# Optimization experiments

Measured on AMD Instinct MI355X. Metric: run time of the kernel, lower is better.

## Reference

```python
import jax, jax.numpy as jnp
import numpy as np

B, N, C, H, HD = 32, 512, 384, 6, 64
WH = WW = WT = 8
ALPHA = 4.0
KS = 5


def safe_pow(x, p):
    # x = relu(...) >= 0; avoid nan grads at x == 0
    pos = x > 0
    return jnp.where(pos, jnp.where(pos, x, 1.0) ** p, 0.0)


def setup_inputs() -> dict:
    key = jax.random.key(0)
    ks = jax.random.split(key, 12)
    s = 0.02
    return {
        "x": jax.random.normal(ks[0], (B, N, C), jnp.float32),
        "y": jax.random.normal(ks[1], (B, N, C), jnp.float32),
        "Wqkvg": jax.random.normal(ks[2], (4 * C, C), jnp.float32) * s,
        "bqkvg": jax.random.normal(ks[3], (4 * C,), jnp.float32) * s,
        "Wproj": jax.random.normal(ks[4], (C, C), jnp.float32) * s,
        "bproj": jax.random.normal(ks[5], (C,), jnp.float32) * s,
        "dwc_w": jax.random.normal(ks[6], (HD, 1, KS, KS, KS), jnp.float32) * s,
        "dwc_b": jax.random.normal(ks[7], (HD,), jnp.float32) * s,
        "power_p": jax.random.normal(ks[8], (1, H, 1, HD), jnp.float32) * s,
        "scale_p": jax.random.normal(ks[9], (1, 1, C), jnp.float32) * s,
        "pe": jax.random.normal(ks[10], (1, N, C), jnp.float32) * s,
    }


def reference(x, y, Wqkvg, bqkvg, Wproj, bproj, dwc_w, dwc_b, power_p, scale_p, pe):
    qkv = (x @ Wqkvg.T + bqkvg).reshape(B, N, 4, C)
    k = qkv[:, :, 1]
    v = qkv[:, :, 2]
    g = qkv[:, :, 3]
    q = (y @ Wqkvg.T + bqkvg).reshape(B, N, 4, C)[:, :, 0]

    k = k + pe
    scale = jax.nn.softplus(scale_p)          # (1,1,C)
    power = 1.0 + ALPHA * jax.nn.sigmoid(power_p)  # (1,H,1,HD)
    q = q / scale
    k = k / scale

    def heads(t):  # (B,N,C) -> (B,H,N,HD)
        return t.reshape(B, N, H, HD).transpose(0, 2, 1, 3)

    q = heads(q)
    k = heads(k)
    v = heads(v)

    q_pos = safe_pow(jax.nn.relu(q), power)
    q_neg = safe_pow(jax.nn.relu(-q), power)
    k_pos = safe_pow(jax.nn.relu(k), power)
    k_neg = safe_pow(jax.nn.relu(-k), power)

    q_sim = jnp.concatenate([q_pos, q_neg], axis=-1)   # (B,H,N,2HD)
    q_opp = jnp.concatenate([q_neg, q_pos], axis=-1)
    kf = jnp.concatenate([k_pos, k_neg], axis=-1)      # (B,H,N,2HD)
    v1, v2 = jnp.split(v, 2, axis=-1)                  # each (B,H,N,HD/2)

    k_mean = kf.mean(axis=-2)                          # (B,H,2HD)
    inv_sqrt_n = N ** (-0.5)
    kfs = kf * inv_sqrt_n

    z_sim = 1.0 / (jnp.einsum("bhnd,bhd->bhn", q_sim, k_mean)[..., None] + 1e-6)
    kv1 = jnp.einsum("bhnd,bhne->bhde", kfs, v1 * inv_sqrt_n)
    x_sim = jnp.einsum("bhnd,bhde->bhne", q_sim, kv1) * z_sim

    z_opp = 1.0 / (jnp.einsum("bhnd,bhd->bhn", q_opp, k_mean)[..., None] + 1e-6)
    kv2 = jnp.einsum("bhnd,bhne->bhde", kfs, v2 * inv_sqrt_n)
    x_opp = jnp.einsum("bhnd,bhde->bhne", q_opp, kv2) * z_opp

    xa = jnp.concatenate([x_sim, x_opp], axis=-1)      # (B,H,N,HD)
    xa = xa.transpose(0, 2, 1, 3).reshape(B, N, C)

    # depthwise conv3d on v: (B*H, HD, Wh, Ww, Wt)
    vr = v.reshape(B * H, WH, WW, WT, HD).transpose(0, 4, 1, 2, 3)
    pad = KS // 2
    vc = jax.lax.conv_general_dilated(
        vr, dwc_w, window_strides=(1, 1, 1),
        padding=[(pad, pad)] * 3,
        dimension_numbers=("NCDHW", "OIDHW", "NCDHW"),
        feature_group_count=HD,
    ) + dwc_b[None, :, None, None, None]
    vc = vc.transpose(0, 2, 3, 4, 1).reshape(B, N, C)

    out = (xa + vc) * g
    out = out @ Wproj.T + bproj
    return out
```

## Files before the change

### kernel.cpp

```cpp
#include <hip/hip_runtime.h>
#include <hip/hip_bf16.h>
#include <math.h>

#define B_  32
#define N_  512
#define C_  384
#define H_  6
#define HD_ 64
#define M_  (B_*N_)

typedef __attribute__((ext_vector_type(8))) short bfrag;
typedef __attribute__((ext_vector_type(8))) unsigned short u16x8;
typedef __attribute__((ext_vector_type(4))) float f32x4;

__device__ __forceinline__ unsigned short f2bfu(float f){
  unsigned int u = __float_as_uint(f);
  u += 0x7fffu + ((u >> 16) & 1u);
  return (unsigned short)(u >> 16);
}
__device__ __forceinline__ float bf2f(unsigned short u){
  return __uint_as_float(((unsigned int)u) << 16);
}
__device__ __forceinline__ bfrag cvt8(float4 a, float4 b){
  bfrag r;
  r[0]=(short)f2bfu(a.x); r[1]=(short)f2bfu(a.y); r[2]=(short)f2bfu(a.z); r[3]=(short)f2bfu(a.w);
  r[4]=(short)f2bfu(b.x); r[5]=(short)f2bfu(b.y); r[6]=(short)f2bfu(b.z); r[7]=(short)f2bfu(b.w);
  return r;
}
__device__ __forceinline__ void gload_lds16(const unsigned short* gp, unsigned short* lp){
  __builtin_amdgcn_global_load_lds(
      (const __attribute__((address_space(1))) void*)gp,
      (__attribute__((address_space(3))) void*)lp, 16, 0, 0);
}

__global__ void param_kernel(const float* __restrict__ scale_p,
                             const float* __restrict__ power_p,
                             float* __restrict__ scale_inv,
                             float* __restrict__ power){
  int t = threadIdx.x;
  if (t < C_){
    float s  = scale_p[t];
    scale_inv[t] = 1.0f / log1pf(expf(s));
  }
  if (t < H_*HD_){
    float p = power_p[t];
    power[t] = 1.0f + 4.0f / (1.0f + expf(-p));
  }
}

__global__ void sentinel_kernel(float* __restrict__ out, int n){
  int i = blockIdx.x*256 + threadIdx.x;
  if (i < n) out[i] = 1.0e9f;
}

__global__ __launch_bounds__(256) void cvt_bf16_kernel(
    const float* __restrict__ x, const float* __restrict__ y,
    const float* __restrict__ W,
    unsigned short* __restrict__ xb, unsigned short* __restrict__ yb,
    unsigned short* __restrict__ Wb)
{
  const int bid = blockIdx.x;
  const float* src; unsigned short* dst; int base;
  if (bid < 3072)      { src = x; dst = xb; base = bid; }
  else if (bid < 6144) { src = y; dst = yb; base = bid - 3072; }
  else                 { src = W; dst = Wb; base = bid - 6144; }
  const size_t i0 = ((size_t)base*256 + threadIdx.x)*8;
  float4 a = *reinterpret_cast<const float4*>(src + i0);
  float4 b = *reinterpret_cast<const float4*>(src + i0 + 4);
  *reinterpret_cast<bfrag*>(dst + i0) = cvt8(a, b);
}

__global__ __launch_bounds__(256) void gemm_qkvg(
    const unsigned short* __restrict__ xb, const unsigned short* __restrict__ yb,
    const unsigned short* __restrict__ Wb, const float* __restrict__ bias,
    const float* __restrict__ pe, const float* __restrict__ scale_inv,
    float* __restrict__ q, float* __restrict__ k,
    unsigned short* __restrict__ v, unsigned short* __restrict__ g)
{
  __shared__ unsigned short As[2][4096];
  __shared__ unsigned short Bs[2][4096];

  const int tid  = threadIdx.x;
  const int row0 = blockIdx.y * 128;
  const int col0 = blockIdx.x * 128;
  const int mode = blockIdx.x / 3;
  const unsigned short* Ab = (mode == 0) ? yb : xb;

  const int wave = tid >> 6, lane = tid & 63;
  const int wm = (wave >> 1) * 64, wn = (wave & 1) * 64;
  const int fr = lane & 15, quad = lane >> 4;
  const int srr = tid >> 2;
  const int skc = (tid & 3) * 8;

  const unsigned short* ga0 = &Ab[(size_t)(row0 + srr)*C_ + skc];
  const unsigned short* gb0 = &Wb[(size_t)(col0 + srr)*C_ + skc];
  const size_t gstep = (size_t)64*C_;

  f32x4 acc[4][4] = {};

  gload_lds16(ga0,         &As[0][tid*8]);
  gload_lds16(ga0 + gstep, &As[0][2048 + tid*8]);
  gload_lds16(gb0,         &Bs[0][tid*8]);
  gload_lds16(gb0 + gstep, &Bs[0][2048 + tid*8]);
  __syncthreads();

  #pragma unroll 2
  for (int t = 0; t < 12; t++){
    const int cur = t & 1;
    if (t < 11){
      const int k0 = (t+1)*32;
      gload_lds16(ga0 + k0,         &As[cur^1][tid*8]);
      gload_lds16(ga0 + gstep + k0, &As[cur^1][2048 + tid*8]);
      gload_lds16(gb0 + k0,         &Bs[cur^1][tid*8]);
      gload_lds16(gb0 + gstep + k0, &Bs[cur^1][2048 + tid*8]);
    }
    bfrag af[4], bf[4];
    #pragma unroll
    for (int f = 0; f < 4; f++){
      af[f] = *reinterpret_cast<const bfrag*>(&As[cur][(wm + f*16 + fr)*32 + quad*8]);
      bf[f] = *reinterpret_cast<const bfrag*>(&Bs[cur][(wn + f*16 + fr)*32 + quad*8]);
    }
    #pragma unroll
    for (int i=0;i<4;i++)
      #pragma unroll
      for (int j=0;j<4;j++)
        acc[i][j] = __builtin_amdgcn_mfma_f32_16x16x32_bf16(af[i], bf[j], acc[i][j], 0, 0, 0);
    __syncthreads();
  }

  const int cbase = col0 - mode*384;
  #pragma unroll
  for (int i = 0; i < 4; i++){
    const int rowb = row0 + wm + i*16 + quad*4;
    #pragma unroll
    for (int j = 0; j < 4; j++){
      const int cc = cbase + wn + j*16 + fr;
      const float bcol = bias[mode*384 + cc];
      if (mode == 0){
        const float scv = scale_inv[cc];
        #pragma unroll
        for (int r = 0; r < 4; r++)
          q[(size_t)(rowb + r)*C_ + cc] = (acc[i][j][r] + bcol) * scv;
      } else if (mode == 1){
        const float scv = scale_inv[cc];
        #pragma unroll
        for (int r = 0; r < 4; r++){
          const int row = rowb + r;
          const int n = row & (N_-1);
          k[(size_t)row*C_ + cc] = (acc[i][j][r] + bcol + pe[n*C_ + cc]) * scv;
        }
      } else if (mode == 2){
        #pragma unroll
        for (int r = 0; r < 4; r++)
          v[(size_t)(rowb + r)*C_ + cc] = f2bfu(acc[i][j][r] + bcol);
      } else {
        #pragma unroll
        for (int r = 0; r < 4; r++)
          g[(size_t)(rowb + r)*C_ + cc] = f2bfu(acc[i][j][r] + bcol);
      }
    }
  }
}

#define NC_ 256
__global__ __launch_bounds__(512) void attn_kernel(
    const float* __restrict__ q, const float* __restrict__ k,
    const unsigned short* __restrict__ v, const float* __restrict__ power,
    float* __restrict__ xa)
{
  const int bh = blockIdx.x;
  const int b = bh / H_, h = bh % H_;
  __shared__ float pw[64];
  __shared__ __align__(16) unsigned short smem[54912];
  unsigned short* kfT  = smem;
  unsigned short* vT   = smem + 33792;
  unsigned short* kvBT = smem;
  unsigned short* qf   = smem + 33792;

  const int tid = threadIdx.x;
  const int wave = tid >> 6, lane = tid & 63;
  const int fr = lane & 15, quad = lane >> 4;
  if (tid < 64) pw[tid] = power[h*HD_ + tid];

  const float*          kbase = k + (size_t)b*N_*C_ + h*HD_;
  const unsigned short* vbase = v + (size_t)b*N_*C_ + h*HD_;

  for (int i = tid; i < 16*NC_; i += 512){
    int e = 64 + (i >> 8);
    int nl = i & (NC_-1);
    vT[e*264 + nl] = (e == 64) ? (unsigned short)0x3F80 : (unsigned short)0;
  }
  __syncthreads();

  f32x4 acc[5] = {};
  for (int chunk = 0; chunk < 2; chunk++){
    const int n0 = chunk * NC_;
    for (int it = 0; it < 32; it++){
      int flat = it*512 + tid;
      int c = flat & 63, nl = flat >> 6;
      float kval = kbase[(size_t)(n0+nl)*C_ + c];
      float p = pw[c];
      float ax = fabsf(kval);
      float pv = (ax > 0.0f) ? exp2f(p * log2f(ax)) : 0.0f;
      kfT[c*264 + nl]      = f2bfu((kval > 0.0f) ? pv : 0.0f);
      kfT[(64+c)*264 + nl] = f2bfu((kval < 0.0f) ? pv : 0.0f);
      vT[c*264 + nl] = vbase[(size_t)(n0+nl)*C_ + c];
    }
    __syncthreads();
    for (int kk = 0; kk < NC_/32; kk++){
      int ko = kk*32 + quad*8;
      bfrag af = *reinterpret_cast<const bfrag*>(&kfT[(wave*16 + fr)*264 + ko]);
      #pragma unroll
      for (int j = 0; j < 5; j++){
        bfrag bf = *reinterpret_cast<const bfrag*>(&vT[(j*16 + fr)*264 + ko]);
        acc[j] = __builtin_amdgcn_mfma_f32_16x16x32_bf16(af, bf, acc[j], 0, 0, 0);
      }
    }
    __syncthreads();
  }

  const float invN = 1.0f / (float)N_;
  {
    const int dbase = wave*16 + quad*4;
    #pragma unroll
    for (int j = 0; j < 4; j++){
      const int e = j*16 + fr;
      const int dd = (e < 32) ? dbase : (dbase ^ 64);
      ushort4 w4;
      w4.x = f2bfu(acc[j][0] * invN);
      w4.y = f2bfu(acc[j][1] * invN);
      w4.z = f2bfu(acc[j][2] * invN);
      w4.w = f2bfu(acc[j][3] * invN);
      *reinterpret_cast<ushort4*>(&kvBT[e*136 + dd]) = w4;
    }
    if (fr == 0){
      ushort4 wk;
      wk.x = f2bfu(acc[4][0] * invN);
      wk.y = f2bfu(acc[4][1] * invN);
      wk.z = f2bfu(acc[4][2] * invN);
      wk.w = f2bfu(acc[4][3] * invN);
      *reinterpret_cast<ushort4*>(&kvBT[64*136 + dbase]) = wk;
      *reinterpret_cast<ushort4*>(&kvBT[65*136 + (dbase^64)]) = wk;
    }
  }
  __syncthreads();

  const float* qbase = q + (size_t)b*N_*C_ + h*HD_;
  float* xabase = xa + (size_t)b*N_*C_ + h*HD_;
  for (int mc = 0; mc < 4; mc++){
    const int m0 = mc * 128;
    for (int it = 0; it < 16; it++){
      int flat = it*512 + tid;
      int c = flat & 63, nl = flat >> 6;
      float qval = qbase[(size_t)(m0+nl)*C_ + c];
      float p = pw[c];
      float ax = fabsf(qval);
      float pv = (ax > 0.0f) ? exp2f(p * log2f(ax)) : 0.0f;
      qf[nl*136 + c]      = f2bfu((qval > 0.0f) ? pv : 0.0f);
      qf[nl*136 + 64 + c] = f2bfu((qval < 0.0f) ? pv : 0.0f);
    }
    __syncthreads();
    f32x4 a2[5] = {};
    for (int kk = 0; kk < 4; kk++){
      int ko = kk*32 + quad*8;
      bfrag af = *reinterpret_cast<const bfrag*>(&qf[(wave*16 + fr)*136 + ko]);
      #pragma unroll
      for (int j = 0; j < 5; j++){
        bfrag bf = *reinterpret_cast<const bfrag*>(&kvBT[(j*16 + fr)*136 + ko]);
        a2[j] = __builtin_amdgcn_mfma_f32_16x16x32_bf16(af, bf, a2[j], 0, 0, 0);
      }
    }
    #pragma unroll
    for (int r = 0; r < 4; r++){
      const float zsim = __shfl(a2[4][r], quad*16);
      const float zopp = __shfl(a2[4][r], quad*16 + 1);
      const int n = m0 + wave*16 + quad*4 + r;
      #pragma unroll
      for (int j = 0; j < 4; j++){
        const int e = j*16 + fr;
        const float z = (e < 32) ? zsim : zopp;
        xabase[(size_t)n*C_ + e] = a2[j][r] / (z + 1e-6f);
      }
    }
    __syncthreads();
  }
}

__global__ __launch_bounds__(512) void conv_kernel(
    const unsigned short* __restrict__ v, const float* __restrict__ dwc_w,
    const float* __restrict__ dwc_b, float* __restrict__ xa)
{
  const int bh = blockIdx.x;
  const int b = bh / H_, h = bh % H_;
  __shared__ float vol[32][521];
  __shared__ float wv[32][126];
  __shared__ float wb[32];
  const int tid = threadIdx.x;
  const unsigned short* vbase = v + (size_t)b*N_*C_ + h*HD_;
  float* xabatch = xa + (size_t)b*N_*C_ + (size_t)h*N_*HD_;

  for (int half = 0; half < 2; half++){
    const int ch0 = half * 32;
    for (int it = 0; it < 32; it++){
      int flat = it*512 + tid;
      int cl = flat & 31, n = flat >> 5;
      vol[cl][n] = bf2f(vbase[(size_t)n*C_ + ch0 + cl]);
    }
    for (int i = tid; i < 32*125; i += 512){
      int ch = i / 125, wi = i - ch*125;
      wv[ch][wi] = dwc_w[(ch0+ch)*125 + wi];
    }
    if (tid < 32) wb[tid] = dwc_b[ch0 + tid];
    __syncthreads();

    for (int t = 0; t < 4; t++){
      const int task = t*512 + tid;
      const int ch = task & 31;
      const int zy = task >> 5;
      const int z = zy >> 3, yc = zy & 7;
      float o[8];
      const float bias = wb[ch];
      #pragma unroll
      for (int xx = 0; xx < 8; xx++) o[xx] = bias;
      #pragma unroll
      for (int kd = 0; kd < 5; kd++){
        const int zz = z + kd - 2;
        if ((unsigned)zz >= 8u) continue;
        #pragma unroll
        for (int kh = 0; kh < 5; kh++){
          const int yy = yc + kh - 2;
          if ((unsigned)yy >= 8u) continue;
          const float* row = &vol[ch][zz*64 + yy*8];
          float rr[8];
          #pragma unroll
          for (int xx = 0; xx < 8; xx++) rr[xx] = row[xx];
          const float* wrow = &wv[ch][kd*25 + kh*5];
          float w5[5];
          #pragma unroll
          for (int kw = 0; kw < 5; kw++) w5[kw] = wrow[kw];
          #pragma unroll
          for (int xx = 0; xx < 8; xx++){
            #pragma unroll
            for (int kw = 0; kw < 5; kw++){
              const int xi = xx + kw - 2;
              if ((unsigned)xi < 8u) o[xx] = fmaf(w5[kw], rr[xi], o[xx]);
            }
          }
        }
      }
      const int nb = zy * 8;
      #pragma unroll
      for (int xx = 0; xx < 8; xx++){
        const size_t di = (size_t)(nb + xx)*HD_ + ch0 + ch;
        xabatch[di] += o[xx];
      }
    }
    __syncthreads();
  }
}

__global__ __launch_bounds__(256) void proj_kernel(
    const float* __restrict__ xa, const unsigned short* __restrict__ g,
    const float* __restrict__ Wp, const float* __restrict__ bp,
    float* __restrict__ out)
{
  __shared__ short As[128][40];
  __shared__ short Bs[128][40];

  const int tid  = threadIdx.x;
  const int row0 = blockIdx.y * 128;
  const int col0 = blockIdx.x * 128;
  const int wave = tid >> 6, lane = tid & 63;
  const int wm = (wave >> 1) * 64, wn = (wave & 1) * 64;
  const int fr = lane & 15, quad = lane >> 4;
  const int sr = tid >> 2;
  const int sk = (tid & 3) * 8;

  f32x4 acc[4][4] = {};

  for (int k0 = 0; k0 < C_; k0 += 32){
    #pragma unroll
    for (int half = 0; half < 2; half++){
      const int r = sr + half*64;
      const size_t aidx = (size_t)(row0 + r)*C_ + k0 + sk;
      float4 x0 = *reinterpret_cast<const float4*>(&xa[aidx]);
      float4 x1 = *reinterpret_cast<const float4*>(&xa[aidx + 4]);
      u16x8 gv = *reinterpret_cast<const u16x8*>(&g[aidx]);
      x0.x*=bf2f(gv[0]); x0.y*=bf2f(gv[1]); x0.z*=bf2f(gv[2]); x0.w*=bf2f(gv[3]);
      x1.x*=bf2f(gv[4]); x1.y*=bf2f(gv[5]); x1.z*=bf2f(gv[6]); x1.w*=bf2f(gv[7]);
      const float* bp2 = &Wp[(size_t)(col0 + r)*C_ + k0 + sk];
      float4 b0 = *reinterpret_cast<const float4*>(bp2);
      float4 b1 = *reinterpret_cast<const float4*>(bp2 + 4);
      *reinterpret_cast<bfrag*>(&As[r][sk]) = cvt8(x0, x1);
      *reinterpret_cast<bfrag*>(&Bs[r][sk]) = cvt8(b0, b1);
    }
    __syncthreads();
    bfrag af[4], bf[4];
    #pragma unroll
    for (int f = 0; f < 4; f++){
      af[f] = *reinterpret_cast<const bfrag*>(&As[wm + f*16 + fr][quad*8]);
      bf[f] = *reinterpret_cast<const bfrag*>(&Bs[wn + f*16 + fr][quad*8]);
    }
    #pragma unroll
    for (int i=0;i<4;i++)
      #pragma unroll
      for (int j=0;j<4;j++)
        acc[i][j] = __builtin_amdgcn_mfma_f32_16x16x32_bf16(af[i], bf[j], acc[i][j], 0, 0, 0);
    __syncthreads();
  }

  #pragma unroll
  for (int i = 0; i < 4; i++){
    const int rowb = row0 + wm + i*16 + quad*4;
    #pragma unroll
    for (int j = 0; j < 4; j++){
      const int col = col0 + wn + j*16 + fr;
      const float bcol = bp[col];
      #pragma unroll
      for (int r = 0; r < 4; r++){
        out[(size_t)(rowb + r)*C_ + col] = acc[i][j][r] + bcol;
      }
    }
  }
}

extern "C" void kernel_launch(void* const* d_in, const int* in_sizes, int n_in,
                              void* d_out, int out_size, void* d_ws, size_t ws_size,
                              hipStream_t stream){
  float* out = (float*)d_out;

  const int expect[11] = {6291456, 6291456, 589824, 1536, 147456, 384, 8000, 64, 384, 384, 196608};
  bool ok = (n_in == 11);
  for (int i = 0; ok && i < 11; i++) ok = (in_sizes[i] == expect[i]);
  if (!ok){
    sentinel_kernel<<<(out_size+255)/256, 256, 0, stream>>>(out, out_size);
    return;
  }

  const float* x    = (const float*)d_in[0];
  const float* y    = (const float*)d_in[1];
  const float* W    = (const float*)d_in[2];
  const float* bq   = (const float*)d_in[3];
  const float* Wp   = (const float*)d_in[4];
  const float* bp   = (const float*)d_in[5];
  const float* dwcw = (const float*)d_in[6];
  const float* dwcb = (const float*)d_in[7];
  const float* pwp  = (const float*)d_in[8];
  const float* scp  = (const float*)d_in[9];
  const float* pe   = (const float*)d_in[10];

  float* ws = (float*)d_ws;
  const size_t SZ = (size_t)M_ * C_;
  float* q  = ws;
  float* k  = ws + SZ;
  unsigned short* v = (unsigned short*)(ws + 2*SZ);
  unsigned short* g = v + SZ;
  float* xa = ws + 3*SZ;
  unsigned short* Wb = (unsigned short*)xa;
  unsigned short* xb = (unsigned short*)(ws + 4*SZ);
  unsigned short* yb = xb + SZ;
  float* scale_inv = ws + 5*SZ;
  float* power     = scale_inv + 512;

  param_kernel<<<1, 512, 0, stream>>>(scp, pwp, scale_inv, power);
  cvt_bf16_kernel<<<6432, 256, 0, stream>>>(x, y, W, xb, yb, Wb);
  gemm_qkvg<<<dim3(12, 128), 256, 0, stream>>>(xb, yb, Wb, bq, pe, scale_inv, q, k, v, g);
  attn_kernel<<<dim3(B_*H_), 512, 0, stream>>>(q, k, v, power, xa);
  conv_kernel<<<dim3(B_*H_), 512, 0, stream>>>(v, dwcw, dwcb, xa);
  proj_kernel<<<dim3(3, 128), 256, 0, stream>>>(xa, g, Wp, bp, out);
}
```

Baseline: 257.2 us.

## Fuse power feature map into QKV GEMM epilogue and bf16 pipeline projection

The QKV GEMM epilogue now applies the scale, positional embedding and signed power feature map directly and writes q/k feature maps as bf16 in a per-head [pos|neg] layout. The attention kernel then only does vectorized copies into shared memory instead of the fp32 loads and per-element pow. The conv kernel fuses the gating multiply and writes a bf16 activation. The projection GEMM uses a pre-converted bf16 Wproj with double-buffered direct-to-LDS loads. This cuts fp32 traffic and repeated transcendental work, at the cost of more complex workspace aliasing and an epilogue that writes twice the q/k elements.

```diff
diff --git a/kernel.cpp b/kernel.cpp
--- a/kernel.cpp
+++ b/kernel.cpp
@@ -55,26 +55,28 @@
 
 __global__ __launch_bounds__(256) void cvt_bf16_kernel(
     const float* __restrict__ x, const float* __restrict__ y,
-    const float* __restrict__ W,
+    const float* __restrict__ W, const float* __restrict__ Wp,
     unsigned short* __restrict__ xb, unsigned short* __restrict__ yb,
-    unsigned short* __restrict__ Wb)
+    unsigned short* __restrict__ Wb, unsigned short* __restrict__ Wpb)
 {
   const int bid = blockIdx.x;
   const float* src; unsigned short* dst; int base;
-  if (bid < 3072)      { src = x; dst = xb; base = bid; }
-  else if (bid < 6144) { src = y; dst = yb; base = bid - 3072; }
-  else                 { src = W; dst = Wb; base = bid - 6144; }
+  if (bid < 3072)      { src = x;  dst = xb;  base = bid; }
+  else if (bid < 6144) { src = y;  dst = yb;  base = bid - 3072; }
+  else if (bid < 6432) { src = W;  dst = Wb;  base = bid - 6144; }
+  else                 { src = Wp; dst = Wpb; base = bid - 6432; }
   const size_t i0 = ((size_t)base*256 + threadIdx.x)*8;
   float4 a = *reinterpret_cast<const float4*>(src + i0);
   float4 b = *reinterpret_cast<const float4*>(src + i0 + 4);
   *reinterpret_cast<bfrag*>(dst + i0) = cvt8(a, b);
 }
 
-__global__ __launch_bounds__(256) void gemm_qkvg(
+__global__ __launch_bounds__(256,4) void gemm_qkvg(
     const unsigned short* __restrict__ xb, const unsigned short* __restrict__ yb,
     const unsigned short* __restrict__ Wb, const float* __restrict__ bias,
     const float* __restrict__ pe, const float* __restrict__ scale_inv,
-    float* __restrict__ q, float* __restrict__ k,
+    const float* __restrict__ power,
+    unsigned short* __restrict__ qf, unsigned short* __restrict__ kf,
     unsigned short* __restrict__ v, unsigned short* __restrict__ g)
 {
   __shared__ unsigned short As[2][4096];
@@ -129,34 +131,44 @@
   }
 
   const int cbase = col0 - mode*384;
-  #pragma unroll
-  for (int i = 0; i < 4; i++){
-    const int rowb = row0 + wm + i*16 + quad*4;
-    #pragma unroll
-    for (int j = 0; j < 4; j++){
-      const int cc = cbase + wn + j*16 + fr;
-      const float bcol = bias[mode*384 + cc];
-      if (mode == 0){
-        const float scv = scale_inv[cc];
-        #pragma unroll
-        for (int r = 0; r < 4; r++)
-          q[(size_t)(rowb + r)*C_ + cc] = (acc[i][j][r] + bcol) * scv;
-      } else if (mode == 1){
-        const float scv = scale_inv[cc];
+  if (mode <= 1){
+    unsigned short* dst = (mode == 0) ? qf : kf;
+    #pragma unroll
+    for (int i = 0; i < 4; i++){
+      const int rowb = row0 + wm + i*16 + quad*4;
+      #pragma unroll
+      for (int j = 0; j < 4; j++){
+        const int cc = cbase + wn + j*16 + fr;
+        const int hh = cc >> 6, dd = cc & 63;
+        const float bcol = bias[mode*384 + cc];
+        const float scv  = scale_inv[cc];
+        const float p    = power[cc];
         #pragma unroll
         for (int r = 0; r < 4; r++){
           const int row = rowb + r;
-          const int n = row & (N_-1);
-          k[(size_t)row*C_ + cc] = (acc[i][j][r] + bcol + pe[n*C_ + cc]) * scv;
+          float val = acc[i][j][r] + bcol;
+          if (mode == 1) val += pe[(row & (N_-1))*C_ + cc];
+          val *= scv;
+          const float ax = fabsf(val);
+          const float pv = (ax > 0.0f) ? exp2f(p * log2f(ax)) : 0.0f;
+          const size_t o = (size_t)row*768 + hh*128 + dd;
+          dst[o]      = f2bfu((val > 0.0f) ? pv : 0.0f);
+          dst[o + 64] = f2bfu((val < 0.0f) ? pv : 0.0f);
         }
-      } else if (mode == 2){
+      }
+    }
+  } else {
+    unsigned short* dst = (mode == 2) ? v : g;
+    #pragma unroll
+    for (int i = 0; i < 4; i++){
+      const int rowb = row0 + wm + i*16 + quad*4;
+      #pragma unroll
+      for (int j = 0; j < 4; j++){
+        const int cc = cbase + wn + j*16 + fr;
+        const float bcol = bias[mode*384 + cc];
         #pragma unroll
         for (int r = 0; r < 4; r++)
-          v[(size_t)(rowb + r)*C_ + cc] = f2bfu(acc[i][j][r] + bcol);
-      } else {
-        #pragma unroll
-        for (int r = 0; r < 4; r++)
-          g[(size_t)(rowb + r)*C_ + cc] = f2bfu(acc[i][j][r] + bcol);
+          dst[(size_t)(rowb + r)*C_ + cc] = f2bfu(acc[i][j][r] + bcol);
       }
     }
   }
@@ -164,26 +176,23 @@
 
 #define NC_ 256
 __global__ __launch_bounds__(512) void attn_kernel(
-    const float* __restrict__ q, const float* __restrict__ k,
-    const unsigned short* __restrict__ v, const float* __restrict__ power,
-    float* __restrict__ xa)
+    const unsigned short* __restrict__ qf, const unsigned short* __restrict__ kf,
+    const unsigned short* __restrict__ v, float* __restrict__ xa)
 {
   const int bh = blockIdx.x;
   const int b = bh / H_, h = bh % H_;
-  __shared__ float pw[64];
   __shared__ __align__(16) unsigned short smem[54912];
   unsigned short* kfT  = smem;
   unsigned short* vT   = smem + 33792;
   unsigned short* kvBT = smem;
-  unsigned short* qf   = smem + 33792;
+  unsigned short* qs   = smem + 33792;
 
   const int tid = threadIdx.x;
   const int wave = tid >> 6, lane = tid & 63;
   const int fr = lane & 15, quad = lane >> 4;
-  if (tid < 64) pw[tid] = power[h*HD_ + tid];
-
-  const float*          kbase = k + (size_t)b*N_*C_ + h*HD_;
-  const unsigned short* vbase = v + (size_t)b*N_*C_ + h*HD_;
+
+  const unsigned short* kfg   = kf + (size_t)b*N_*768 + h*128;
+  const unsigned short* vbase = v  + (size_t)b*N_*C_  + h*HD_;
 
   for (int i = tid; i < 16*NC_; i += 512){
     int e = 64 + (i >> 8);
@@ -195,16 +204,19 @@
   f32x4 acc[5] = {};
   for (int chunk = 0; chunk < 2; chunk++){
     const int n0 = chunk * NC_;
-    for (int it = 0; it < 32; it++){
+    for (int it = 0; it < 8; it++){
       int flat = it*512 + tid;
-      int c = flat & 63, nl = flat >> 6;
-      float kval = kbase[(size_t)(n0+nl)*C_ + c];
-      float p = pw[c];
-      float ax = fabsf(kval);
-      float pv = (ax > 0.0f) ? exp2f(p * log2f(ax)) : 0.0f;
-      kfT[c*264 + nl]      = f2bfu((kval > 0.0f) ? pv : 0.0f);
-      kfT[(64+c)*264 + nl] = f2bfu((kval < 0.0f) ? pv : 0.0f);
-      vT[c*264 + nl] = vbase[(size_t)(n0+nl)*C_ + c];
+      int cg = flat & 15, nl = flat >> 4;
+      u16x8 k8 = *reinterpret_cast<const u16x8*>(&kfg[(size_t)(n0+nl)*768 + cg*8]);
+      #pragma unroll
+      for (int j = 0; j < 8; j++) kfT[(cg*8+j)*264 + nl] = k8[j];
+    }
+    for (int it = 0; it < 4; it++){
+      int flat = it*512 + tid;
+      int cg = flat & 7, nl = flat >> 3;
+      u16x8 v8 = *reinterpret_cast<const u16x8*>(&vbase[(size_t)(n0+nl)*C_ + cg*8]);
+      #pragma unroll
+      for (int j = 0; j < 8; j++) vT[(cg*8+j)*264 + nl] = v8[j];
     }
     __syncthreads();
     for (int kk = 0; kk < NC_/32; kk++){
@@ -245,25 +257,21 @@
   }
   __syncthreads();
 
-  const float* qbase = q + (size_t)b*N_*C_ + h*HD_;
+  const unsigned short* qfg = qf + (size_t)b*N_*768 + h*128;
   float* xabase = xa + (size_t)b*N_*C_ + h*HD_;
   for (int mc = 0; mc < 4; mc++){
     const int m0 = mc * 128;
-    for (int it = 0; it < 16; it++){
+    for (int it = 0; it < 4; it++){
       int flat = it*512 + tid;
-      int c = flat & 63, nl = flat >> 6;
-      float qval = qbase[(size_t)(m0+nl)*C_ + c];
-      float p = pw[c];
-      float ax = fabsf(qval);
-      float pv = (ax > 0.0f) ? exp2f(p * log2f(ax)) : 0.0f;
-      qf[nl*136 + c]      = f2bfu((qval > 0.0f) ? pv : 0.0f);
-      qf[nl*136 + 64 + c] = f2bfu((qval < 0.0f) ? pv : 0.0f);
+      int cg = flat & 15, nl = flat >> 4;
+      *reinterpret_cast<u16x8*>(&qs[nl*136 + cg*8]) =
+          *reinterpret_cast<const u16x8*>(&qfg[(size_t)(m0+nl)*768 + cg*8]);
     }
     __syncthreads();
     f32x4 a2[5] = {};
     for (int kk = 0; kk < 4; kk++){
       int ko = kk*32 + quad*8;
-      bfrag af = *reinterpret_cast<const bfrag*>(&qf[(wave*16 + fr)*136 + ko]);
+      bfrag af = *reinterpret_cast<const bfrag*>(&qs[(wave*16 + fr)*136 + ko]);
       #pragma unroll
       for (int j = 0; j < 5; j++){
         bfrag bf = *reinterpret_cast<const bfrag*>(&kvBT[(j*16 + fr)*136 + ko]);
@@ -288,7 +296,8 @@
 
 __global__ __launch_bounds__(512) void conv_kernel(
     const unsigned short* __restrict__ v, const float* __restrict__ dwc_w,
-    const float* __restrict__ dwc_b, float* __restrict__ xa)
+    const float* __restrict__ dwc_b, const float* __restrict__ xa,
+    const unsigned short* __restrict__ g, unsigned short* __restrict__ ab)
 {
   const int bh = blockIdx.x;
   const int b = bh / H_, h = bh % H_;
@@ -297,7 +306,9 @@
   __shared__ float wb[32];
   const int tid = threadIdx.x;
   const unsigned short* vbase = v + (size_t)b*N_*C_ + h*HD_;
-  float* xabatch = xa + (size_t)b*N_*C_ + (size_t)h*N_*HD_;
+  const float* xabatch = xa + (size_t)b*N_*C_ + (size_t)h*N_*HD_;
+  const unsigned short* gb = g + (size_t)b*N_*C_ + (size_t)h*N_*HD_;
+  unsigned short* abb = ab + (size_t)b*N_*C_ + (size_t)h*N_*HD_;
 
   for (int half = 0; half < 2; half++){
     const int ch0 = half * 32;
@@ -352,20 +363,19 @@
       #pragma unroll
       for (int xx = 0; xx < 8; xx++){
         const size_t di = (size_t)(nb + xx)*HD_ + ch0 + ch;
-        xabatch[di] += o[xx];
-      }
-    }
-    __syncthreads();
-  }
-}
-
-__global__ __launch_bounds__(256) void proj_kernel(
-    const float* __restrict__ xa, const unsigned short* __restrict__ g,
-    const float* __restrict__ Wp, const float* __restrict__ bp,
-    float* __restrict__ out)
+        abb[di] = f2bfu((xabatch[di] + o[xx]) * bf2f(gb[di]));
+      }
+    }
+    __syncthreads();
+  }
+}
+
+__global__ __launch_bounds__(256,4) void proj_kernel(
+    const unsigned short* __restrict__ ab, const unsigned short* __restrict__ Wpb,
+    const float* __restrict__ bp, float* __restrict__ out)
 {
-  __shared__ short As[128][40];
-  __shared__ short Bs[128][40];
+  __shared__ unsigned short As[2][4096];
+  __shared__ unsigned short Bs[2][4096];
 
   const int tid  = threadIdx.x;
   const int row0 = blockIdx.y * 128;
@@ -373,33 +383,36 @@
   const int wave = tid >> 6, lane = tid & 63;
   const int wm = (wave >> 1) * 64, wn = (wave & 1) * 64;
   const int fr = lane & 15, quad = lane >> 4;
-  const int sr = tid >> 2;
-  const int sk = (tid & 3) * 8;
+  const int srr = tid >> 2;
+  const int skc = (tid & 3) * 8;
+
+  const unsigned short* ga0 = &ab[(size_t)(row0 + srr)*C_ + skc];
+  const unsigned short* gb0 = &Wpb[(size_t)(col0 + srr)*C_ + skc];
+  const size_t gstep = (size_t)64*C_;
 
   f32x4 acc[4][4] = {};
 
-  for (int k0 = 0; k0 < C_; k0 += 32){
-    #pragma unroll
-    for (int half = 0; half < 2; half++){
-      const int r = sr + half*64;
-      const size_t aidx = (size_t)(row0 + r)*C_ + k0 + sk;
-      float4 x0 = *reinterpret_cast<const float4*>(&xa[aidx]);
-      float4 x1 = *reinterpret_cast<const float4*>(&xa[aidx + 4]);
-      u16x8 gv = *reinterpret_cast<const u16x8*>(&g[aidx]);
-      x0.x*=bf2f(gv[0]); x0.y*=bf2f(gv[1]); x0.z*=bf2f(gv[2]); x0.w*=bf2f(gv[3]);
-      x1.x*=bf2f(gv[4]); x1.y*=bf2f(gv[5]); x1.z*=bf2f(gv[6]); x1.w*=bf2f(gv[7]);
-      const float* bp2 = &Wp[(size_t)(col0 + r)*C_ + k0 + sk];
-      float4 b0 = *reinterpret_cast<const float4*>(bp2);
-      float4 b1 = *reinterpret_cast<const float4*>(bp2 + 4);
-      *reinterpret_cast<bfrag*>(&As[r][sk]) = cvt8(x0, x1);
-      *reinterpret_cast<bfrag*>(&Bs[r][sk]) = cvt8(b0, b1);
-    }
-    __syncthreads();
+  gload_lds16(ga0,         &As[0][tid*8]);
+  gload_lds16(ga0 + gstep, &As[0][2048 + tid*8]);
+  gload_lds16(gb0,         &Bs[0][tid*8]);
+  gload_lds16(gb0 + gstep, &Bs[0][2048 + tid*8]);
+  __syncthreads();
+
+  #pragma unroll 2
+  for (int t = 0; t < 12; t++){
+    const int cur = t & 1;
+    if (t < 11){
+      const int k0 = (t+1)*32;
+      gload_lds16(ga0 + k0,         &As[cur^1][tid*8]);
+      gload_lds16(ga0 + gstep + k0, &As[cur^1][2048 + tid*8]);
+      gload_lds16(gb0 + k0,         &Bs[cur^1][tid*8]);
+      gload_lds16(gb0 + gstep + k0, &Bs[cur^1][2048 + tid*8]);
+    }
     bfrag af[4], bf[4];
     #pragma unroll
     for (int f = 0; f < 4; f++){
-      af[f] = *reinterpret_cast<const bfrag*>(&As[wm + f*16 + fr][quad*8]);
-      bf[f] = *reinterpret_cast<const bfrag*>(&Bs[wn + f*16 + fr][quad*8]);
+      af[f] = *reinterpret_cast<const bfrag*>(&As[cur][(wm + f*16 + fr)*32 + quad*8]);
+      bf[f] = *reinterpret_cast<const bfrag*>(&Bs[cur][(wn + f*16 + fr)*32 + quad*8]);
     }
     #pragma unroll
     for (int i=0;i<4;i++)
@@ -417,9 +430,8 @@
       const int col = col0 + wn + j*16 + fr;
       const float bcol = bp[col];
       #pragma unroll
-      for (int r = 0; r < 4; r++){
+      for (int r = 0; r < 4; r++)
         out[(size_t)(rowb + r)*C_ + col] = acc[i][j][r] + bcol;
-      }
     }
   }
 }
@@ -451,21 +463,23 @@
 
   float* ws = (float*)d_ws;
   const size_t SZ = (size_t)M_ * C_;
-  float* q  = ws;
-  float* k  = ws + SZ;
-  unsigned short* v = (unsigned short*)(ws + 2*SZ);
-  unsigned short* g = v + SZ;
+  unsigned short* qf  = (unsigned short*)ws;
+  unsigned short* kfb = qf + 2*SZ;
+  unsigned short* v   = (unsigned short*)(ws + 2*SZ);
+  unsigned short* g   = v + SZ;
+  unsigned short* xb  = (unsigned short*)(ws + 3*SZ);
+  unsigned short* yb  = xb + SZ;
   float* xa = ws + 3*SZ;
-  unsigned short* Wb = (unsigned short*)xa;
-  unsigned short* xb = (unsigned short*)(ws + 4*SZ);
-  unsigned short* yb = xb + SZ;
-  float* scale_inv = ws + 5*SZ;
+  unsigned short* ab  = (unsigned short*)ws;
+  unsigned short* Wb  = (unsigned short*)(ws + 4*SZ);
+  unsigned short* Wpb = Wb + 589824;
+  float* scale_inv = (float*)(Wpb + 147456);
   float* power     = scale_inv + 512;
 
   param_kernel<<<1, 512, 0, stream>>>(scp, pwp, scale_inv, power);
-  cvt_bf16_kernel<<<6432, 256, 0, stream>>>(x, y, W, xb, yb, Wb);
-  gemm_qkvg<<<dim3(12, 128), 256, 0, stream>>>(xb, yb, Wb, bq, pe, scale_inv, q, k, v, g);
-  attn_kernel<<<dim3(B_*H_), 512, 0, stream>>>(q, k, v, power, xa);
-  conv_kernel<<<dim3(B_*H_), 512, 0, stream>>>(v, dwcw, dwcb, xa);
-  proj_kernel<<<dim3(3, 128), 256, 0, stream>>>(xa, g, Wp, bp, out);
-}
+  cvt_bf16_kernel<<<6504, 256, 0, stream>>>(x, y, W, Wp, xb, yb, Wb, Wpb);
+  gemm_qkvg<<<dim3(12, 128), 256, 0, stream>>>(xb, yb, Wb, bq, pe, scale_inv, power, qf, kfb, v, g);
+  attn_kernel<<<dim3(B_*H_), 512, 0, stream>>>(qf, kfb, v, xa);
+  conv_kernel<<<dim3(B_*H_), 512, 0, stream>>>(v, dwcw, dwcb, xa, g, ab);
+  proj_kernel<<<dim3(3, 128), 256, 0, stream>>>(ab, Wpb, bp, out);
+}
```

Result: slower. 267.5 us (+4.0%).
